# Performance work log

Measured on AMD Instinct MI355X. Metric: run time of the kernel, lower is better.

The kernel has to match this reference:

```python
import jax, jax.numpy as jnp
import numpy as np

GRID = 8        # kornia equalize_clahe default grid_size=(8,8)
NUM_BINS = 256  # kornia default
CLIP_LIMIT = 40.0


def normalize_in_range(x, lo, hi):
    mn, mx = x.min(), x.max()
    return (x - mn) / (mx - mn) * (hi - lo) + lo


def equalize_clahe(x, clip_limit=CLIP_LIMIT, grid=GRID, bins=NUM_BINS):
    # x: (B, C, H, W) in [0, 1]; H, W divisible by grid
    B, C, H, W = x.shape
    th, tw = H // grid, W // grid
    pixels = th * tw

    # --- per-pixel bin index (histc with bins=256, min=0, max=1) ---
    bidx = jnp.clip((x * bins).astype(jnp.int32), 0, bins - 1)  # (B,C,H,W)

    # --- per-tile histograms via one segment_sum (scatter-add) ---
    ti = (jnp.arange(H) // th)[None, None, :, None]
    tj = (jnp.arange(W) // tw)[None, None, None, :]
    bb = jnp.arange(B)[:, None, None, None]
    cc = jnp.arange(C)[None, :, None, None]
    tile_id = ((bb * C + cc) * grid + ti) * grid + tj          # (B,C,H,W)
    flat = (tile_id * bins + bidx).reshape(-1)
    hist = jax.ops.segment_sum(
        jnp.ones(flat.shape, jnp.float32), flat,
        num_segments=B * C * grid * grid * bins,
    ).reshape(B, C, grid, grid, bins)

    # --- clip histogram and redistribute excess uniformly ---
    max_val = max(int(clip_limit * pixels // bins), 1)
    hist = jnp.minimum(hist, max_val)
    residual = (pixels - hist.sum(-1, keepdims=True)) / bins
    hist = hist + residual

    # --- CDF -> LUT (values in [0, bins-1], floored) ---
    lut = jnp.floor(jnp.clip(jnp.cumsum(hist, axis=-1) * ((bins - 1) / pixels),
                             0.0, bins - 1.0))                 # (B,C,gh,gw,bins)

    # --- bilinear interpolation between the 4 nearest tile LUTs ---
    gi = jnp.clip((jnp.arange(H) + 0.5) / th - 0.5, 0.0, grid - 1.0)
    gj = jnp.clip((jnp.arange(W) + 0.5) / tw - 0.5, 0.0, grid - 1.0)
    i0 = jnp.floor(gi).astype(jnp.int32); i1 = jnp.minimum(i0 + 1, grid - 1)
    j0 = jnp.floor(gj).astype(jnp.int32); j1 = jnp.minimum(j0 + 1, grid - 1)
    wy = (gi - i0)[None, None, :, None]
    wx = (gj - j0)[None, None, None, :]

    I0 = i0[None, None, :, None]; I1 = i1[None, None, :, None]
    J0 = j0[None, None, None, :]; J1 = j1[None, None, None, :]

    v00 = lut[bb, cc, I0, J0, bidx]
    v01 = lut[bb, cc, I0, J1, bidx]
    v10 = lut[bb, cc, I1, J0, bidx]
    v11 = lut[bb, cc, I1, J1, bidx]

    out = (1.0 - wy) * ((1.0 - wx) * v00 + wx * v01) + wy * ((1.0 - wx) * v10 + wx * v11)
    return out / (bins - 1)


def setup_inputs() -> dict:
    key = jax.random.key(0)
    kx, ky = jax.random.split(key)
    x = jax.random.normal(kx, (16, 1, 1024, 1024), dtype=jnp.float32)
    y = jax.random.randint(ky, (16,), 0, 10, dtype=jnp.int64)
    return {"x": x, "y": y}


def reference(x, y):
    x = normalize_in_range(x, 0.0, 1.0)
    mean = x.mean(axis=(0, 2, 3))
    std = jnp.std(x, axis=(0, 2, 3), ddof=1)  # torch unbiased std
    x = (x - mean[None, :, None, None]) / std[None, :, None, None]
    x = normalize_in_range(x, 0.0, 1.0)
    x = equalize_clahe(x, clip_limit=40.0)
    return (x, y)
```

## Files before the change

### kernel.cpp

```cpp
#include <hip/hip_runtime.h>


#define BINS 256
#define MAXV 2560u

__device__ __forceinline__ unsigned fenc(float f){
  unsigned u = __float_as_uint(f);
  return (u & 0x80000000u) ? ~u : (u | 0x80000000u);
}
__device__ __forceinline__ float fdec(unsigned e){
  unsigned u = (e & 0x80000000u) ? (e & 0x7FFFFFFFu) : ~e;
  return __uint_as_float(u);
}

__global__ void k_init(unsigned* mm, const int* __restrict__ y,
                       float* __restrict__ out, int N, int tail){
  int t = threadIdx.x;
  if (t == 0){ mm[0] = 0xFFFFFFFFu; mm[1] = 0u; }
  if (t < tail) out[N + t] = (float)y[t];
}

__global__ __launch_bounds__(256) void k_minmax(const float4* __restrict__ x4,
                                                unsigned* mm, int n4){
  int tid = blockIdx.x * blockDim.x + threadIdx.x;
  int stride = gridDim.x * blockDim.x;
  float lmin = INFINITY, lmax = -INFINITY;
  for (int i = tid; i < n4; i += stride){
    float4 v = x4[i];
    lmin = fminf(lmin, fminf(fminf(v.x, v.y), fminf(v.z, v.w)));
    lmax = fmaxf(lmax, fmaxf(fmaxf(v.x, v.y), fmaxf(v.z, v.w)));
  }
  for (int o = 32; o > 0; o >>= 1){
    lmin = fminf(lmin, __shfl_down(lmin, o, 64));
    lmax = fmaxf(lmax, __shfl_down(lmax, o, 64));
  }
  __shared__ float smin[4], smax[4];
  int lane = threadIdx.x & 63, wv = threadIdx.x >> 6;
  if (lane == 0){ smin[wv] = lmin; smax[wv] = lmax; }
  __syncthreads();
  if (threadIdx.x == 0){
    float m = smin[0], M = smax[0];
    #pragma unroll
    for (int i = 1; i < 4; i++){ m = fminf(m, smin[i]); M = fmaxf(M, smax[i]); }
    atomicMin(&mm[0], fenc(m));
    atomicMax(&mm[1], fenc(M));
  }
}

__global__ __launch_bounds__(256) void k_hist(const float* __restrict__ x,
                                              const unsigned* __restrict__ mm,
                                              float* __restrict__ lut,
                                              unsigned char* __restrict__ bins){
  __shared__ unsigned hist8[8 * 257];
  __shared__ unsigned wsum[4];
  __shared__ unsigned sc[BINS];
  int t = threadIdx.x;
  for (int i = t; i < 8 * 257; i += 256) hist8[i] = 0u;
  float mn = fdec(mm[0]);
  float inv = 1.0f / (fdec(mm[1]) - mn);
  int tile = blockIdx.x;
  int bc = tile >> 6, ti = (tile >> 3) & 7, tj = tile & 7;
  size_t base = ((size_t)bc * 1024 + ti * 128) * 1024 + tj * 128;
  const float4* x4 = (const float4*)(x + base);
  uchar4* b4 = bins ? (uchar4*)(bins + base) : nullptr;
  unsigned hc = (t & 7) * 257;
  __syncthreads();
  #pragma unroll 4
  for (int k = 0; k < 16; k++){
    int p = t + (k << 8);
    int row = p >> 5, col = p & 31;
    float4 v = x4[row * 256 + col];
    int b0 = min(max((int)(((v.x - mn) * inv) * 256.0f), 0), 255);
    int b1 = min(max((int)(((v.y - mn) * inv) * 256.0f), 0), 255);
    int b2 = min(max((int)(((v.z - mn) * inv) * 256.0f), 0), 255);
    int b3 = min(max((int)(((v.w - mn) * inv) * 256.0f), 0), 255);
    if (b4) b4[row * 256 + col] = make_uchar4((unsigned char)b0, (unsigned char)b1,
                                              (unsigned char)b2, (unsigned char)b3);
    atomicAdd(&hist8[hc + b0], 1u);
    atomicAdd(&hist8[hc + b1], 1u);
    atomicAdd(&hist8[hc + b2], 1u);
    atomicAdd(&hist8[hc + b3], 1u);
  }
  __syncthreads();
  unsigned h = 0;
  #pragma unroll
  for (int c = 0; c < 8; c++) h += hist8[c * 257 + t];
  if (h > MAXV) h = MAXV;
  unsigned s = h;
  for (int o = 32; o > 0; o >>= 1) s += __shfl_down(s, o, 64);
  int lane = t & 63, wv = t >> 6;
  if (lane == 0) wsum[wv] = s;
  __syncthreads();
  unsigned total = wsum[0] + wsum[1] + wsum[2] + wsum[3];
  float residual = (16384.0f - (float)total) * (1.0f / 256.0f);
  sc[t] = h;
  __syncthreads();
  for (int o = 1; o < 256; o <<= 1){
    unsigned v = (t >= o) ? sc[t - o] : 0u;
    __syncthreads();
    sc[t] += v;
    __syncthreads();
  }
  float cum = ((float)sc[t] + (float)(t + 1) * residual) * (255.0f / 16384.0f);
  lut[(size_t)tile * BINS + t] = floorf(fminf(fmaxf(cum, 0.0f), 255.0f));
}

__global__ __launch_bounds__(256) void k_apply(const float* __restrict__ x,
                                               const uchar4* __restrict__ binsq,
                                               const unsigned* __restrict__ mm,
                                               const float* __restrict__ lutg,
                                               float* __restrict__ out){
  __shared__ float l0s[2048];
  __shared__ float l1s[2048];
  int t = threadIdx.x;
  int strip = blockIdx.x;
  int b = strip >> 6;
  int r0 = (strip & 63) << 4;
  float gi = fminf(fmaxf((r0 + 0.5f) * (1.0f / 128.0f) - 0.5f, 0.0f), 7.0f);
  int i0 = (int)gi;
  int i1 = min(i0 + 1, 7);
  const float4* g0 = (const float4*)(lutg + ((size_t)b * 8 + i0) * 2048);
  const float4* g1 = (const float4*)(lutg + ((size_t)b * 8 + i1) * 2048);
  ((float4*)l0s)[t]       = g0[t];
  ((float4*)l0s)[t + 256] = g0[t + 256];
  ((float4*)l1s)[t]       = g1[t];
  ((float4*)l1s)[t + 256] = g1[t + 256];
  int j0[4], j1[4];
  float wx[4];
  #pragma unroll
  for (int c = 0; c < 4; c++){
    int col = (t << 2) + c;
    float gj = fminf(fmaxf((col + 0.5f) * (1.0f / 128.0f) - 0.5f, 0.0f), 7.0f);
    j0[c] = (int)gj;
    j1[c] = min(j0[c] + 1, 7);
    wx[c] = gj - (float)j0[c];
  }
  float mn = 0.0f, inv = 0.0f;
  if (!binsq){ mn = fdec(mm[0]); inv = 1.0f / (fdec(mm[1]) - mn); }
  size_t base4 = ((size_t)b * 1024 + r0) * 256;
  __syncthreads();
  for (int r = 0; r < 16; r++){
    int h = r0 + r;
    float giw = fminf(fmaxf((h + 0.5f) * (1.0f / 128.0f) - 0.5f, 0.0f), 7.0f);
    float wy = giw - (float)i0;
    int bi[4];
    if (binsq){
      uchar4 bv = binsq[base4 + r * 256 + t];
      bi[0] = bv.x; bi[1] = bv.y; bi[2] = bv.z; bi[3] = bv.w;
    } else {
      float4 xv = ((const float4*)x)[base4 + r * 256 + t];
      bi[0] = min(max((int)(((xv.x - mn) * inv) * 256.0f), 0), 255);
      bi[1] = min(max((int)(((xv.y - mn) * inv) * 256.0f), 0), 255);
      bi[2] = min(max((int)(((xv.z - mn) * inv) * 256.0f), 0), 255);
      bi[3] = min(max((int)(((xv.w - mn) * inv) * 256.0f), 0), 255);
    }
    float res[4];
    #pragma unroll
    for (int c = 0; c < 4; c++){
      float v00 = l0s[(j0[c] << 8) + bi[c]];
      float v01 = l0s[(j1[c] << 8) + bi[c]];
      float v10 = l1s[(j0[c] << 8) + bi[c]];
      float v11 = l1s[(j1[c] << 8) + bi[c]];
      float top = v00 + wx[c] * (v01 - v00);
      float bot = v10 + wx[c] * (v11 - v10);
      res[c] = (top + wy * (bot - top)) * (1.0f / 255.0f);
    }
    ((float4*)out)[base4 + r * 256 + t] = make_float4(res[0], res[1], res[2], res[3]);
  }
}

extern "C" void kernel_launch(void* const* d_in, const int* in_sizes, int n_in,
                              void* d_out, int out_size, void* d_ws, size_t ws_size,
                              hipStream_t stream){
  const float* x = (const float*)d_in[0];
  const int* y = (const int*)d_in[1];
  float* out = (float*)d_out;
  int N = in_sizes[0];
  int B = N >> 20;
  int n4 = N >> 2;
  unsigned* mm = (unsigned*)d_ws;
  float* lut = (float*)((char*)d_ws + 256);
  size_t lutbytes = (size_t)B * 64 * 256 * 4;
  unsigned char* bins = (unsigned char*)d_ws + 256 + lutbytes;
  bool use_bins = ws_size >= 256 + lutbytes + (size_t)N;
  int tail = out_size - N;

  hipLaunchKernelGGL(k_init, dim3(1), dim3(64), 0, stream, mm, y, out, N, tail);
  hipLaunchKernelGGL(k_minmax, dim3(1024), dim3(256), 0, stream,
                     (const float4*)x, mm, n4);
  hipLaunchKernelGGL(k_hist, dim3(B * 64), dim3(256), 0, stream,
                     x, mm, lut, use_bins ? bins : nullptr);
  hipLaunchKernelGGL(k_apply, dim3(B * 64), dim3(256), 0, stream,
                     x, use_bins ? (const uchar4*)bins : nullptr, mm, lut, out);
}
```

Before: 156.7 us.

## Fuse minmax, histogram and apply into one persistent kernel with grid barriers

Replaces the three separate kernels with one kernel that loads each tile into registers once, computes the global min/max, then builds the histogram and LUT from those registers, with software grid barriers between phases. This avoids reading x twice from global memory and saves two kernel launches. All 1024 blocks must be co-resident for the spin barriers to work. Launch bounds of 4 blocks per CU and roughly 25KB of shared memory per block are meant to allow that, but the code does not check it and would deadlock if co-residency fails. The path that recomputed bins when the workspace was too small is also removed.

```diff
diff --git a/kernel.cpp b/kernel.cpp
--- a/kernel.cpp
+++ b/kernel.cpp
@@ -16,66 +16,73 @@
 __global__ void k_init(unsigned* mm, const int* __restrict__ y,
                        float* __restrict__ out, int N, int tail){
   int t = threadIdx.x;
-  if (t == 0){ mm[0] = 0xFFFFFFFFu; mm[1] = 0u; }
+  if (t == 0){ mm[0] = 0xFFFFFFFFu; mm[1] = 0u; mm[2] = 0u; mm[3] = 0u; }
   if (t < tail) out[N + t] = (float)y[t];
 }
 
-__global__ __launch_bounds__(256) void k_minmax(const float4* __restrict__ x4,
-                                                unsigned* mm, int n4){
-  int tid = blockIdx.x * blockDim.x + threadIdx.x;
-  int stride = gridDim.x * blockDim.x;
+__device__ __forceinline__ void gridbar(unsigned* bar, unsigned nb){
+  __syncthreads();
+  if (threadIdx.x == 0){
+    __threadfence();
+    __hip_atomic_fetch_add(bar, 1u, __ATOMIC_ACQ_REL, __HIP_MEMORY_SCOPE_AGENT);
+    while (__hip_atomic_load(bar, __ATOMIC_ACQUIRE, __HIP_MEMORY_SCOPE_AGENT) < nb)
+      __builtin_amdgcn_s_sleep(8);
+  }
+  __syncthreads();
+}
+
+__global__ __launch_bounds__(256, 4)
+void k_fused(const float* __restrict__ x, unsigned* mm,
+             float* __restrict__ lutg, unsigned char* __restrict__ bins,
+             float* __restrict__ out){
+  __shared__ unsigned hist8[8 * 257 + 260];
+  __shared__ float l01[4096];
+  int t = threadIdx.x;
+  int tile = blockIdx.x;
+  unsigned nb = gridDim.x;
+  int bc = tile >> 6, ti = (tile >> 3) & 7, tj = tile & 7;
+  size_t tbase = ((size_t)bc * 1024 + ti * 128) * 1024 + tj * 128;
+  const float4* x4 = (const float4*)(x + tbase);
+
+  float4 v[16];
+  #pragma unroll
+  for (int k = 0; k < 16; k++){
+    int p = t + (k << 8);
+    v[k] = x4[(p >> 5) * 256 + (p & 31)];
+  }
   float lmin = INFINITY, lmax = -INFINITY;
-  for (int i = tid; i < n4; i += stride){
-    float4 v = x4[i];
-    lmin = fminf(lmin, fminf(fminf(v.x, v.y), fminf(v.z, v.w)));
-    lmax = fmaxf(lmax, fmaxf(fmaxf(v.x, v.y), fmaxf(v.z, v.w)));
+  #pragma unroll
+  for (int k = 0; k < 16; k++){
+    lmin = fminf(lmin, fminf(fminf(v[k].x, v[k].y), fminf(v[k].z, v[k].w)));
+    lmax = fmaxf(lmax, fmaxf(fmaxf(v[k].x, v[k].y), fmaxf(v[k].z, v[k].w)));
   }
   for (int o = 32; o > 0; o >>= 1){
     lmin = fminf(lmin, __shfl_down(lmin, o, 64));
     lmax = fmaxf(lmax, __shfl_down(lmax, o, 64));
   }
-  __shared__ float smin[4], smax[4];
-  int lane = threadIdx.x & 63, wv = threadIdx.x >> 6;
-  if (lane == 0){ smin[wv] = lmin; smax[wv] = lmax; }
+  if ((t & 63) == 0){
+    atomicMin(&mm[0], fenc(lmin));
+    atomicMax(&mm[1], fenc(lmax));
+  }
+  gridbar(&mm[2], nb);
+
+  for (int i = t; i < 8 * 257; i += 256) hist8[i] = 0u;
   __syncthreads();
-  if (threadIdx.x == 0){
-    float m = smin[0], M = smax[0];
-    #pragma unroll
-    for (int i = 1; i < 4; i++){ m = fminf(m, smin[i]); M = fmaxf(M, smax[i]); }
-    atomicMin(&mm[0], fenc(m));
-    atomicMax(&mm[1], fenc(M));
-  }
-}
-
-__global__ __launch_bounds__(256) void k_hist(const float* __restrict__ x,
-                                              const unsigned* __restrict__ mm,
-                                              float* __restrict__ lut,
-                                              unsigned char* __restrict__ bins){
-  __shared__ unsigned hist8[8 * 257];
-  __shared__ unsigned wsum[4];
-  __shared__ unsigned sc[BINS];
-  int t = threadIdx.x;
-  for (int i = t; i < 8 * 257; i += 256) hist8[i] = 0u;
-  float mn = fdec(mm[0]);
-  float inv = 1.0f / (fdec(mm[1]) - mn);
-  int tile = blockIdx.x;
-  int bc = tile >> 6, ti = (tile >> 3) & 7, tj = tile & 7;
-  size_t base = ((size_t)bc * 1024 + ti * 128) * 1024 + tj * 128;
-  const float4* x4 = (const float4*)(x + base);
-  uchar4* b4 = bins ? (uchar4*)(bins + base) : nullptr;
+  float mn = fdec(__hip_atomic_load(&mm[0], __ATOMIC_RELAXED, __HIP_MEMORY_SCOPE_AGENT));
+  float mx = fdec(__hip_atomic_load(&mm[1], __ATOMIC_RELAXED, __HIP_MEMORY_SCOPE_AGENT));
+  float inv = 1.0f / (mx - mn);
+  uchar4* b4 = (uchar4*)(bins + tbase);
   unsigned hc = (t & 7) * 257;
-  __syncthreads();
   #pragma unroll 4
   for (int k = 0; k < 16; k++){
     int p = t + (k << 8);
     int row = p >> 5, col = p & 31;
-    float4 v = x4[row * 256 + col];
-    int b0 = min(max((int)(((v.x - mn) * inv) * 256.0f), 0), 255);
-    int b1 = min(max((int)(((v.y - mn) * inv) * 256.0f), 0), 255);
-    int b2 = min(max((int)(((v.z - mn) * inv) * 256.0f), 0), 255);
-    int b3 = min(max((int)(((v.w - mn) * inv) * 256.0f), 0), 255);
-    if (b4) b4[row * 256 + col] = make_uchar4((unsigned char)b0, (unsigned char)b1,
-                                              (unsigned char)b2, (unsigned char)b3);
+    int b0 = min(max((int)(((v[k].x - mn) * inv) * 256.0f), 0), 255);
+    int b1 = min(max((int)(((v[k].y - mn) * inv) * 256.0f), 0), 255);
+    int b2 = min(max((int)(((v[k].z - mn) * inv) * 256.0f), 0), 255);
+    int b3 = min(max((int)(((v[k].w - mn) * inv) * 256.0f), 0), 255);
+    b4[row * 256 + col] = make_uchar4((unsigned char)b0, (unsigned char)b1,
+                                      (unsigned char)b2, (unsigned char)b3);
     atomicAdd(&hist8[hc + b0], 1u);
     atomicAdd(&hist8[hc + b1], 1u);
     atomicAdd(&hist8[hc + b2], 1u);
@@ -86,39 +93,33 @@
   #pragma unroll
   for (int c = 0; c < 8; c++) h += hist8[c * 257 + t];
   if (h > MAXV) h = MAXV;
+  unsigned* sc = hist8 + 8 * 257;
+  unsigned* wsum = sc + 256;
   unsigned s = h;
   for (int o = 32; o > 0; o >>= 1) s += __shfl_down(s, o, 64);
-  int lane = t & 63, wv = t >> 6;
-  if (lane == 0) wsum[wv] = s;
+  if ((t & 63) == 0) wsum[t >> 6] = s;
   __syncthreads();
   unsigned total = wsum[0] + wsum[1] + wsum[2] + wsum[3];
   float residual = (16384.0f - (float)total) * (1.0f / 256.0f);
   sc[t] = h;
   __syncthreads();
   for (int o = 1; o < 256; o <<= 1){
-    unsigned v = (t >= o) ? sc[t - o] : 0u;
+    unsigned pv = (t >= o) ? sc[t - o] : 0u;
     __syncthreads();
-    sc[t] += v;
+    sc[t] += pv;
     __syncthreads();
   }
   float cum = ((float)sc[t] + (float)(t + 1) * residual) * (255.0f / 16384.0f);
-  lut[(size_t)tile * BINS + t] = floorf(fminf(fmaxf(cum, 0.0f), 255.0f));
-}
+  lutg[(size_t)tile * BINS + t] = floorf(fminf(fmaxf(cum, 0.0f), 255.0f));
+  gridbar(&mm[3], nb);
 
-__global__ __launch_bounds__(256) void k_apply(const float* __restrict__ x,
-                                               const uchar4* __restrict__ binsq,
-                                               const unsigned* __restrict__ mm,
-                                               const float* __restrict__ lutg,
-                                               float* __restrict__ out){
-  __shared__ float l0s[2048];
-  __shared__ float l1s[2048];
-  int t = threadIdx.x;
-  int strip = blockIdx.x;
-  int b = strip >> 6;
-  int r0 = (strip & 63) << 4;
+  int b = tile >> 6;
+  int r0 = (tile & 63) << 4;
   float gi = fminf(fmaxf((r0 + 0.5f) * (1.0f / 128.0f) - 0.5f, 0.0f), 7.0f);
   int i0 = (int)gi;
   int i1 = min(i0 + 1, 7);
+  float* l0s = l01;
+  float* l1s = l01 + 2048;
   const float4* g0 = (const float4*)(lutg + ((size_t)b * 8 + i0) * 2048);
   const float4* g1 = (const float4*)(lutg + ((size_t)b * 8 + i1) * 2048);
   ((float4*)l0s)[t]       = g0[t];
@@ -135,25 +136,15 @@
     j1[c] = min(j0[c] + 1, 7);
     wx[c] = gj - (float)j0[c];
   }
-  float mn = 0.0f, inv = 0.0f;
-  if (!binsq){ mn = fdec(mm[0]); inv = 1.0f / (fdec(mm[1]) - mn); }
   size_t base4 = ((size_t)b * 1024 + r0) * 256;
+  const uchar4* binsq = (const uchar4*)bins;
   __syncthreads();
   for (int r = 0; r < 16; r++){
-    int h = r0 + r;
-    float giw = fminf(fmaxf((h + 0.5f) * (1.0f / 128.0f) - 0.5f, 0.0f), 7.0f);
+    int hh = r0 + r;
+    float giw = fminf(fmaxf((hh + 0.5f) * (1.0f / 128.0f) - 0.5f, 0.0f), 7.0f);
     float wy = giw - (float)i0;
-    int bi[4];
-    if (binsq){
-      uchar4 bv = binsq[base4 + r * 256 + t];
-      bi[0] = bv.x; bi[1] = bv.y; bi[2] = bv.z; bi[3] = bv.w;
-    } else {
-      float4 xv = ((const float4*)x)[base4 + r * 256 + t];
-      bi[0] = min(max((int)(((xv.x - mn) * inv) * 256.0f), 0), 255);
-      bi[1] = min(max((int)(((xv.y - mn) * inv) * 256.0f), 0), 255);
-      bi[2] = min(max((int)(((xv.z - mn) * inv) * 256.0f), 0), 255);
-      bi[3] = min(max((int)(((xv.w - mn) * inv) * 256.0f), 0), 255);
-    }
+    uchar4 bv = binsq[base4 + r * 256 + t];
+    int bi[4] = {bv.x, bv.y, bv.z, bv.w};
     float res[4];
     #pragma unroll
     for (int c = 0; c < 4; c++){
@@ -177,19 +168,13 @@
   float* out = (float*)d_out;
   int N = in_sizes[0];
   int B = N >> 20;
-  int n4 = N >> 2;
   unsigned* mm = (unsigned*)d_ws;
   float* lut = (float*)((char*)d_ws + 256);
   size_t lutbytes = (size_t)B * 64 * 256 * 4;
   unsigned char* bins = (unsigned char*)d_ws + 256 + lutbytes;
-  bool use_bins = ws_size >= 256 + lutbytes + (size_t)N;
   int tail = out_size - N;
 
   hipLaunchKernelGGL(k_init, dim3(1), dim3(64), 0, stream, mm, y, out, N, tail);
-  hipLaunchKernelGGL(k_minmax, dim3(1024), dim3(256), 0, stream,
-                     (const float4*)x, mm, n4);
-  hipLaunchKernelGGL(k_hist, dim3(B * 64), dim3(256), 0, stream,
-                     x, mm, lut, use_bins ? bins : nullptr);
-  hipLaunchKernelGGL(k_apply, dim3(B * 64), dim3(256), 0, stream,
-                     x, use_bins ? (const uchar4*)bins : nullptr, mm, lut, out);
+  hipLaunchKernelGGL(k_fused, dim3(B * 64), dim3(256), 0, stream,
+                     x, mm, lut, bins, out);
 }
```

Result: slower. 604.3 us (+285.8%).
